# Optimization experiments

Measured on AMD Instinct MI355X. Metric: run time of the kernel, lower is better.

Reference implementation:

```python
import jax, jax.numpy as jnp
import numpy as np


def setup_inputs() -> dict:
    key = jax.random.key(0)
    k1, k2 = jax.random.split(key)
    x = jax.random.normal(k1, (32, 256, 56, 56), dtype=jnp.float32)
    # Conv2d(2 -> 1, kernel 7x7, bias=False): weight [out_c=1, in_c=2, 7, 7]
    w_conv = jax.random.normal(k2, (1, 2, 7, 7), dtype=jnp.float32) * 0.1
    return {"x": x, "w_conv": w_conv}


def reference(x, w_conv):
    # channel-wise average and max pooling -> [B, 2, H, W]
    avgout = jnp.mean(x, axis=1, keepdims=True)
    maxout = jnp.max(x, axis=1, keepdims=True)
    x1 = jnp.concatenate([avgout, maxout], axis=1)
    # 7x7 conv, padding=3 (SAME), NCHW / OIHW
    x1 = jax.lax.conv_general_dilated(
        x1, w_conv,
        window_strides=(1, 1),
        padding=((3, 3), (3, 3)),
        dimension_numbers=("NCHW", "OIHW", "NCHW"),
    )
    gate = jax.nn.sigmoid(x1)  # [B, 1, H, W]
    return x * gate
```

## Files before the change

kernel.cpp:

```cpp
#include <hip/hip_runtime.h>
#include <math.h>

#define B_    32
#define C_    256
#define H_    56
#define W_    56
#define HW_   (H_ * W_)
#define BHW_  (B_ * HW_)
#define HW4_  (HW_ / 4)
#define NF4_  (BHW_ / 4)
#define GRID_ 1568
#define CHUNKF4_ (NF4_ / GRID_)
#define POSPB_  (BHW_ / GRID_)

typedef float f4v __attribute__((ext_vector_type(4)));

__global__ __launch_bounds__(256) void sa_reduce_kernel(
    const float* __restrict__ x, float* __restrict__ pool) {
  const int t = threadIdx.x;
  const int lane = t & 15;
  const int cgrp = t >> 4;
  const unsigned if4 = (unsigned)blockIdx.x * CHUNKF4_ + lane;
  const unsigned bimg = if4 / HW4_;
  const unsigned hw4 = if4 % HW4_;
  const f4v* __restrict__ x4 = (const f4v*)x;
  const unsigned base = (bimg * C_ + cgrp) * HW4_ + hw4;

  f4v s = {0.f, 0.f, 0.f, 0.f};
  f4v m = {-INFINITY, -INFINITY, -INFINITY, -INFINITY};
#pragma unroll 8
  for (int k = 0; k < 16; ++k) {
    f4v v = x4[base + (unsigned)(k * 16) * HW4_];
    s += v;
    m = (f4v){fmaxf(m.x, v.x), fmaxf(m.y, v.y),
              fmaxf(m.z, v.z), fmaxf(m.w, v.w)};
  }

  __shared__ f4v ssum[16][16];
  __shared__ f4v smax[16][16];
  ssum[cgrp][lane] = s;
  smax[cgrp][lane] = m;
  __syncthreads();

  if (t < 16) {
    f4v S = ssum[0][t];
    f4v M = smax[0][t];
#pragma unroll
    for (int g = 1; g < 16; ++g) {
      f4v sg = ssum[g][t];
      f4v mg = smax[g][t];
      S += sg;
      M = (f4v){fmaxf(M.x, mg.x), fmaxf(M.y, mg.y),
                fmaxf(M.z, mg.z), fmaxf(M.w, mg.w)};
    }
    f4v* p4 = (f4v*)pool;
    const unsigned jf4 = (unsigned)blockIdx.x * CHUNKF4_ + t;
    const unsigned bb = jf4 / HW4_;
    const unsigned hh = jf4 % HW4_;
    p4[bb * 2 * HW4_ + hh]        = S * (1.0f / (float)C_);
    p4[bb * 2 * HW4_ + HW4_ + hh] = M;
  }
}

__global__ __launch_bounds__(256) void sa_conv_apply_kernel(
    const float* __restrict__ x, const float* __restrict__ pool,
    const float* __restrict__ wt, float* __restrict__ out) {
  const int t = threadIdx.x;
  __shared__ float partial[128];
  __shared__ f4v sgate4[CHUNKF4_];

  if (t < 2 * POSPB_) {
    const int pos = t >> 1;
    const int ic = t & 1;
    const unsigned p = (unsigned)blockIdx.x * POSPB_ + (unsigned)pos;
    const unsigned bimg = p / HW_;
    const unsigned hw = p % HW_;
    const int h = (int)(hw / W_);
    const int w = (int)(hw % W_);
    const float* pl = pool + ((long)bimg * 2 + ic) * HW_;
    const float* wr0 = wt + ic * 49;
    float acc = 0.f;
#pragma unroll
    for (int kh = 0; kh < 7; ++kh) {
      const int ih = h + kh - 3;
      if (ih < 0 || ih >= H_) continue;
      const float* row = pl + ih * W_;
      const float* wr = wr0 + kh * 7;
#pragma unroll
      for (int kw = 0; kw < 7; ++kw) {
        const int iw = w + kw - 3;
        if (iw < 0 || iw >= W_) continue;
        acc = fmaf(row[iw], wr[kw], acc);
      }
    }
    partial[t] = acc;
  }
  __syncthreads();
  if (t < POSPB_) {
    float a = partial[2 * t] + partial[2 * t + 1];
    ((float*)sgate4)[t] = 1.0f / (1.0f + __expf(-a));
  }
  __syncthreads();

  const int lane = t & 15;
  const int cgrp = t >> 4;
  const unsigned if4 = (unsigned)blockIdx.x * CHUNKF4_ + lane;
  const unsigned bimg = if4 / HW4_;
  const unsigned hw4 = if4 % HW4_;
  const unsigned base = (bimg * C_ + cgrp) * HW4_ + hw4;
  const f4v* __restrict__ x4 = (const f4v*)x;
  f4v* __restrict__ o4 = (f4v*)out;
  const f4v g = sgate4[lane];
#pragma unroll 8
  for (int k = 0; k < 16; ++k) {
    const unsigned idx = base + (unsigned)(k * 16) * HW4_;
    f4v v = x4[idx];
    __builtin_nontemporal_store(v * g, &o4[idx]);
  }
}

extern "C" void kernel_launch(void* const* d_in, const int* in_sizes, int n_in,
                              void* d_out, int out_size, void* d_ws, size_t ws_size,
                              hipStream_t stream) {
  const float* x  = (const float*)d_in[0];
  const float* wc = (const float*)d_in[1];
  float* out = (float*)d_out;
  float* pool = (float*)d_ws;

  sa_reduce_kernel<<<GRID_, 256, 0, stream>>>(x, pool);
  sa_conv_apply_kernel<<<GRID_, 256, 0, stream>>>(x, pool, wc, out);
}
```

Before: 202.3 us.

## Double block size, widen spatial chunk, split conv rows across four threads

Halves the grid and doubles threads per block, so each block covers 128 contiguous float4 positions (32 lanes) instead of 64. Each thread now walks 16 consecutive channels instead of channels strided by 16. The 7x7 conv is split over four threads per output position (two input channels times two kernel-row halves), which keeps all 512 threads busy and shortens the serial conv prologue before the apply loop. Launch bounds request 6 blocks per CU, which may constrain registers. Each wave now reads a 512-byte contiguous run per channel row, slightly shorter than the 256-byte runs... actually wider than before.

After: 208.4 us. 1.03x slower.

```diff
diff --git a/kernel.cpp b/kernel.cpp
--- a/kernel.cpp
+++ b/kernel.cpp
@@ -9,40 +9,40 @@
 #define BHW_  (B_ * HW_)
 #define HW4_  (HW_ / 4)
 #define NF4_  (BHW_ / 4)
-#define GRID_ 1568
+#define GRID_ 784
 #define CHUNKF4_ (NF4_ / GRID_)
 #define POSPB_  (BHW_ / GRID_)
 
 typedef float f4v __attribute__((ext_vector_type(4)));
 
-__global__ __launch_bounds__(256) void sa_reduce_kernel(
+__global__ __launch_bounds__(512, 6) void sa_reduce_kernel(
     const float* __restrict__ x, float* __restrict__ pool) {
   const int t = threadIdx.x;
-  const int lane = t & 15;
-  const int cgrp = t >> 4;
+  const int lane = t & 31;
+  const int cgrp = t >> 5;
   const unsigned if4 = (unsigned)blockIdx.x * CHUNKF4_ + lane;
   const unsigned bimg = if4 / HW4_;
   const unsigned hw4 = if4 % HW4_;
   const f4v* __restrict__ x4 = (const f4v*)x;
-  const unsigned base = (bimg * C_ + cgrp) * HW4_ + hw4;
+  const unsigned base = (bimg * C_ + cgrp * 16) * HW4_ + hw4;
 
   f4v s = {0.f, 0.f, 0.f, 0.f};
   f4v m = {-INFINITY, -INFINITY, -INFINITY, -INFINITY};
 #pragma unroll 8
   for (int k = 0; k < 16; ++k) {
-    f4v v = x4[base + (unsigned)(k * 16) * HW4_];
+    f4v v = x4[base + (unsigned)k * HW4_];
     s += v;
     m = (f4v){fmaxf(m.x, v.x), fmaxf(m.y, v.y),
               fmaxf(m.z, v.z), fmaxf(m.w, v.w)};
   }
 
-  __shared__ f4v ssum[16][16];
-  __shared__ f4v smax[16][16];
+  __shared__ f4v ssum[16][32];
+  __shared__ f4v smax[16][32];
   ssum[cgrp][lane] = s;
   smax[cgrp][lane] = m;
   __syncthreads();
 
-  if (t < 16) {
+  if (t < 32) {
     f4v S = ssum[0][t];
     f4v M = smax[0][t];
 #pragma unroll
@@ -62,26 +62,29 @@
   }
 }
 
-__global__ __launch_bounds__(256) void sa_conv_apply_kernel(
+__global__ __launch_bounds__(512, 6) void sa_conv_apply_kernel(
     const float* __restrict__ x, const float* __restrict__ pool,
     const float* __restrict__ wt, float* __restrict__ out) {
   const int t = threadIdx.x;
-  __shared__ float partial[128];
+  __shared__ float partial[512];
   __shared__ f4v sgate4[CHUNKF4_];
 
-  if (t < 2 * POSPB_) {
-    const int pos = t >> 1;
-    const int ic = t & 1;
+  {
+    const int pos = t >> 2;
+    const int sub = t & 3;
+    const int ic = sub & 1;
+    const int khalf = sub >> 1;
     const unsigned p = (unsigned)blockIdx.x * POSPB_ + (unsigned)pos;
-    const unsigned bimg = p / HW_;
+    const unsigned bimg_a = p / HW_;
     const unsigned hw = p % HW_;
     const int h = (int)(hw / W_);
     const int w = (int)(hw % W_);
-    const float* pl = pool + ((long)bimg * 2 + ic) * HW_;
+    const float* pl = pool + ((long)bimg_a * 2 + ic) * HW_;
     const float* wr0 = wt + ic * 49;
+    const int kh0 = khalf ? 4 : 0;
+    const int kh1 = khalf ? 7 : 4;
     float acc = 0.f;
-#pragma unroll
-    for (int kh = 0; kh < 7; ++kh) {
+    for (int kh = kh0; kh < kh1; ++kh) {
       const int ih = h + kh - 3;
       if (ih < 0 || ih >= H_) continue;
       const float* row = pl + ih * W_;
@@ -97,23 +100,24 @@
   }
   __syncthreads();
   if (t < POSPB_) {
-    float a = partial[2 * t] + partial[2 * t + 1];
+    float a = partial[4 * t] + partial[4 * t + 1] +
+              partial[4 * t + 2] + partial[4 * t + 3];
     ((float*)sgate4)[t] = 1.0f / (1.0f + __expf(-a));
   }
   __syncthreads();
 
-  const int lane = t & 15;
-  const int cgrp = t >> 4;
+  const int lane = t & 31;
+  const int cgrp = t >> 5;
   const unsigned if4 = (unsigned)blockIdx.x * CHUNKF4_ + lane;
   const unsigned bimg = if4 / HW4_;
   const unsigned hw4 = if4 % HW4_;
-  const unsigned base = (bimg * C_ + cgrp) * HW4_ + hw4;
+  const unsigned base = (bimg * C_ + cgrp * 16) * HW4_ + hw4;
   const f4v* __restrict__ x4 = (const f4v*)x;
   f4v* __restrict__ o4 = (f4v*)out;
   const f4v g = sgate4[lane];
 #pragma unroll 8
   for (int k = 0; k < 16; ++k) {
-    const unsigned idx = base + (unsigned)(k * 16) * HW4_;
+    const unsigned idx = base + (unsigned)k * HW4_;
     f4v v = x4[idx];
     __builtin_nontemporal_store(v * g, &o4[idx]);
   }
@@ -127,6 +131,6 @@
   float* out = (float*)d_out;
   float* pool = (float*)d_ws;
 
-  sa_reduce_kernel<<<GRID_, 256, 0, stream>>>(x, pool);
-  sa_conv_apply_kernel<<<GRID_, 256, 0, stream>>>(x, pool, wc, out);
+  sa_reduce_kernel<<<GRID_, 512, 0, stream>>>(x, pool);
+  sa_conv_apply_kernel<<<GRID_, 512, 0, stream>>>(x, pool, wc, out);
 }
```

## Split pooling into partial reduce, combine+conv, and contiguous apply kernels

Applied to the files above, without the earlier changes.

Replaces the two-kernel pipeline with three kernels. The first produces partial channel sums and maxes over groups of 8 channels. The second combines the partials and computes the 7x7 conv and sigmoid from shared-memory tiles. The third applies the gate using fully contiguous 4096-float4 chunks per block, with the gate map staged in LDS. The aim is to make loads coalesced and contiguous rather than strided across channels, and to stop recomputing the conv redundantly, at the cost of an extra launch and about 25 MB of partial writes and reads. It falls back to the old path if the workspace is too small.

Measured after the change: 209.2 us. 3.4% more time.

```diff
diff --git a/kernel.cpp b/kernel.cpp
--- a/kernel.cpp
+++ b/kernel.cpp
@@ -5,60 +5,200 @@
 #define C_    256
 #define H_    56
 #define W_    56
-#define HW_   (H_ * W_)
-#define BHW_  (B_ * HW_)
-#define HW4_  (HW_ / 4)
-#define NF4_  (BHW_ / 4)
-#define GRID_ 1568
-#define CHUNKF4_ (NF4_ / GRID_)
-#define POSPB_  (BHW_ / GRID_)
+#define HW_   3136
+#define HW4_  784
+#define NF4_  (B_ * C_ * HW4_)
 
 typedef float f4v __attribute__((ext_vector_type(4)));
+
+static __device__ __forceinline__ f4v f4max(f4v a, f4v b) {
+  return (f4v){fmaxf(a.x, b.x), fmaxf(a.y, b.y), fmaxf(a.z, b.z), fmaxf(a.w, b.w)};
+}
+
+
+__global__ __launch_bounds__(256, 4) void k1_partial(
+    const float* __restrict__ x, float* __restrict__ part) {
+  const int t = threadIdx.x;
+  const unsigned k = blockIdx.x;
+  const unsigned img = k >> 5;
+  const unsigned grp = k & 31u;
+  const f4v* __restrict__ x4 = (const f4v*)x;
+  f4v* __restrict__ p4 = (f4v*)part;
+  const unsigned xbase = (img * 256u + grp * 8u) * 784u;
+  const int w = t >> 6;
+  const int l = t & 63;
+
+#pragma unroll
+  for (int it = 0; it < 4; ++it) {
+    const int off = it * 64 + l;
+    if (off < 196) {
+      const unsigned q = 196u * (unsigned)w + (unsigned)off;
+      f4v v0 = x4[xbase + 0u * 784u + q];
+      f4v v1 = x4[xbase + 1u * 784u + q];
+      f4v v2 = x4[xbase + 2u * 784u + q];
+      f4v v3 = x4[xbase + 3u * 784u + q];
+      f4v v4 = x4[xbase + 4u * 784u + q];
+      f4v v5 = x4[xbase + 5u * 784u + q];
+      f4v v6 = x4[xbase + 6u * 784u + q];
+      f4v v7 = x4[xbase + 7u * 784u + q];
+      f4v s = ((v0 + v1) + (v2 + v3)) + ((v4 + v5) + (v6 + v7));
+      f4v m = f4max(f4max(f4max(v0, v1), f4max(v2, v3)),
+                    f4max(f4max(v4, v5), f4max(v6, v7)));
+      p4[k * 1568u + q]        = s;
+      p4[k * 1568u + 784u + q] = m;
+    }
+  }
+}
+
+__global__ __launch_bounds__(256) void k1b_combine_conv(
+    const float* __restrict__ part, const float* __restrict__ wt,
+    float* __restrict__ gate) {
+  const int t = threadIdx.x;
+  const unsigned blk = blockIdx.x;
+  const unsigned img = blk / 7u;
+  const int r0 = (int)(blk % 7u) * 8;
+
+  __shared__ float lsum[784];
+  __shared__ float lmax[784];
+  const f4v* __restrict__ p4 = (const f4v*)part;
+
+  for (int s = t; s < 392; s += 256) {
+    const int is_max = (s >= 196);
+    const int sl = is_max ? (s - 196) : s;
+    const int lr = sl / 14;
+    const int c  = sl % 14;
+    const int row = r0 - 3 + lr;
+    f4v acc;
+    if (row < 0 || row >= 56) {
+      acc = (f4v){0.f, 0.f, 0.f, 0.f};
+    } else {
+      const unsigned qq = (unsigned)(row * 14 + c);
+      if (!is_max) {
+        f4v a = {0.f, 0.f, 0.f, 0.f};
+#pragma unroll 8
+        for (int g = 0; g < 32; ++g)
+          a += p4[(img * 32u + (unsigned)g) * 1568u + qq];
+        acc = a * (1.0f / 256.0f);
+      } else {
+        f4v a = {-INFINITY, -INFINITY, -INFINITY, -INFINITY};
+#pragma unroll 8
+        for (int g = 0; g < 32; ++g)
+          a = f4max(a, p4[(img * 32u + (unsigned)g) * 1568u + 784u + qq]);
+        acc = a;
+      }
+    }
+    ((f4v*)(is_max ? lmax : lsum))[sl] = acc;
+  }
+  __syncthreads();
+
+  const float* __restrict__ w0 = wt;
+  const float* __restrict__ w1 = wt + 49;
+#pragma unroll
+  for (int pp = 0; pp < 2; ++pp) {
+    const int pos = t + 256 * pp;
+    if (pos < 448) {
+      const int lro = pos / 56;
+      const int wc = pos % 56;
+      float a = 0.f;
+#pragma unroll
+      for (int kh = 0; kh < 7; ++kh) {
+        const float* rs = lsum + (lro + kh) * 56;
+        const float* rm = lmax + (lro + kh) * 56;
+        const float* t0 = w0 + kh * 7;
+        const float* t1 = w1 + kh * 7;
+#pragma unroll
+        for (int kw = 0; kw < 7; ++kw) {
+          const int iw = wc + kw - 3;
+          if (iw >= 0 && iw < 56) {
+            a = fmaf(rs[iw], t0[kw], a);
+            a = fmaf(rm[iw], t1[kw], a);
+          }
+        }
+      }
+      gate[img * 3136u + (unsigned)(r0 + lro) * 56u + (unsigned)wc] =
+          1.0f / (1.0f + __expf(-a));
+    }
+  }
+}
+
+__global__ __launch_bounds__(256) void k2_apply(
+    const float* __restrict__ x, const float* __restrict__ gate,
+    float* __restrict__ out) {
+  const int t = threadIdx.x;
+  const unsigned k = blockIdx.x;
+  const unsigned img = k / 49u;
+  const unsigned S = (176u * (k % 49u)) % 784u;
+
+  __shared__ f4v lg[784];
+  const f4v* __restrict__ g4 = (const f4v*)gate;
+#pragma unroll
+  for (int it = 0; it < 4; ++it) {
+    const int idx = t + 256 * it;
+    if (idx < 784) lg[idx] = g4[img * 784u + (unsigned)idx];
+  }
+  __syncthreads();
+
+  const f4v* __restrict__ x4 = (const f4v*)x;
+  f4v* __restrict__ o4 = (f4v*)out;
+  const unsigned base = k * 4096u + (unsigned)t;
+  unsigned qc = S + (unsigned)t;
+  if (qc >= 784u) qc -= 784u;
+
+#pragma unroll
+  for (int hb = 0; hb < 2; ++hb) {
+    f4v v[8];
+#pragma unroll
+    for (int u = 0; u < 8; ++u)
+      v[u] = x4[base + (unsigned)(hb * 8 + u) * 256u];
+#pragma unroll
+    for (int u = 0; u < 8; ++u) {
+      const f4v g = lg[qc];
+      __builtin_nontemporal_store(v[u] * g,
+                                  &o4[base + (unsigned)(hb * 8 + u) * 256u]);
+      qc += 256u;
+      if (qc >= 784u) qc -= 784u;
+    }
+  }
+}
 
 __global__ __launch_bounds__(256) void sa_reduce_kernel(
     const float* __restrict__ x, float* __restrict__ pool) {
   const int t = threadIdx.x;
   const int lane = t & 15;
   const int cgrp = t >> 4;
-  const unsigned if4 = (unsigned)blockIdx.x * CHUNKF4_ + lane;
-  const unsigned bimg = if4 / HW4_;
-  const unsigned hw4 = if4 % HW4_;
-  const f4v* __restrict__ x4 = (const f4v*)x;
-  const unsigned base = (bimg * C_ + cgrp) * HW4_ + hw4;
+  const unsigned if4 = (unsigned)blockIdx.x * 16u + (unsigned)lane;
+  const unsigned bimg = if4 / 784u;
+  const unsigned hw4 = if4 % 784u;
+  const f4v* __restrict__ x4 = (const f4v*)x;
+  const unsigned base = (bimg * 256u + (unsigned)cgrp) * 784u + hw4;
 
   f4v s = {0.f, 0.f, 0.f, 0.f};
   f4v m = {-INFINITY, -INFINITY, -INFINITY, -INFINITY};
 #pragma unroll 8
-  for (int k = 0; k < 16; ++k) {
-    f4v v = x4[base + (unsigned)(k * 16) * HW4_];
+  for (int kk = 0; kk < 16; ++kk) {
+    f4v v = x4[base + (unsigned)(kk * 16) * 784u];
     s += v;
-    m = (f4v){fmaxf(m.x, v.x), fmaxf(m.y, v.y),
-              fmaxf(m.z, v.z), fmaxf(m.w, v.w)};
-  }
-
+    m = f4max(m, v);
+  }
   __shared__ f4v ssum[16][16];
   __shared__ f4v smax[16][16];
   ssum[cgrp][lane] = s;
   smax[cgrp][lane] = m;
   __syncthreads();
-
   if (t < 16) {
     f4v S = ssum[0][t];
     f4v M = smax[0][t];
 #pragma unroll
     for (int g = 1; g < 16; ++g) {
-      f4v sg = ssum[g][t];
-      f4v mg = smax[g][t];
-      S += sg;
-      M = (f4v){fmaxf(M.x, mg.x), fmaxf(M.y, mg.y),
-                fmaxf(M.z, mg.z), fmaxf(M.w, mg.w)};
+      S += ssum[g][t];
+      M = f4max(M, smax[g][t]);
     }
     f4v* p4 = (f4v*)pool;
-    const unsigned jf4 = (unsigned)blockIdx.x * CHUNKF4_ + t;
-    const unsigned bb = jf4 / HW4_;
-    const unsigned hh = jf4 % HW4_;
-    p4[bb * 2 * HW4_ + hh]        = S * (1.0f / (float)C_);
-    p4[bb * 2 * HW4_ + HW4_ + hh] = M;
+    const unsigned jf4 = (unsigned)blockIdx.x * 16u + (unsigned)t;
+    const unsigned bb = jf4 / 784u;
+    const unsigned hh = jf4 % 784u;
+    p4[bb * 1568u + hh]        = S * (1.0f / 256.0f);
+    p4[bb * 1568u + 784u + hh] = M;
   }
 }
 
@@ -67,36 +207,35 @@
     const float* __restrict__ wt, float* __restrict__ out) {
   const int t = threadIdx.x;
   __shared__ float partial[128];
-  __shared__ f4v sgate4[CHUNKF4_];
-
-  if (t < 2 * POSPB_) {
+  __shared__ f4v sgate4[16];
+  if (t < 128) {
     const int pos = t >> 1;
     const int ic = t & 1;
-    const unsigned p = (unsigned)blockIdx.x * POSPB_ + (unsigned)pos;
-    const unsigned bimg = p / HW_;
-    const unsigned hw = p % HW_;
-    const int h = (int)(hw / W_);
-    const int w = (int)(hw % W_);
-    const float* pl = pool + ((long)bimg * 2 + ic) * HW_;
+    const unsigned p = (unsigned)blockIdx.x * 64u + (unsigned)pos;
+    const unsigned bimg = p / 3136u;
+    const unsigned hw = p % 3136u;
+    const int h = (int)(hw / 56u);
+    const int w = (int)(hw % 56u);
+    const float* pl = pool + ((long)bimg * 2 + ic) * 3136;
     const float* wr0 = wt + ic * 49;
     float acc = 0.f;
 #pragma unroll
     for (int kh = 0; kh < 7; ++kh) {
       const int ih = h + kh - 3;
-      if (ih < 0 || ih >= H_) continue;
-      const float* row = pl + ih * W_;
+      if (ih < 0 || ih >= 56) continue;
+      const float* row = pl + ih * 56;
       const float* wr = wr0 + kh * 7;
 #pragma unroll
       for (int kw = 0; kw < 7; ++kw) {
         const int iw = w + kw - 3;
-        if (iw < 0 || iw >= W_) continue;
+        if (iw < 0 || iw >= 56) continue;
         acc = fmaf(row[iw], wr[kw], acc);
       }
     }
     partial[t] = acc;
   }
   __syncthreads();
-  if (t < POSPB_) {
+  if (t < 64) {
     float a = partial[2 * t] + partial[2 * t + 1];
     ((float*)sgate4)[t] = 1.0f / (1.0f + __expf(-a));
   }
@@ -104,16 +243,16 @@
 
   const int lane = t & 15;
   const int cgrp = t >> 4;
-  const unsigned if4 = (unsigned)blockIdx.x * CHUNKF4_ + lane;
-  const unsigned bimg = if4 / HW4_;
-  const unsigned hw4 = if4 % HW4_;
-  const unsigned base = (bimg * C_ + cgrp) * HW4_ + hw4;
+  const unsigned if4 = (unsigned)blockIdx.x * 16u + (unsigned)lane;
+  const unsigned bimg = if4 / 784u;
+  const unsigned hw4 = if4 % 784u;
+  const unsigned base = (bimg * 256u + (unsigned)cgrp) * 784u + hw4;
   const f4v* __restrict__ x4 = (const f4v*)x;
   f4v* __restrict__ o4 = (f4v*)out;
   const f4v g = sgate4[lane];
 #pragma unroll 8
-  for (int k = 0; k < 16; ++k) {
-    const unsigned idx = base + (unsigned)(k * 16) * HW4_;
+  for (int kk = 0; kk < 16; ++kk) {
+    const unsigned idx = base + (unsigned)(kk * 16) * 784u;
     f4v v = x4[idx];
     __builtin_nontemporal_store(v * g, &o4[idx]);
   }
@@ -125,8 +264,20 @@
   const float* x  = (const float*)d_in[0];
   const float* wc = (const float*)d_in[1];
   float* out = (float*)d_out;
-  float* pool = (float*)d_ws;
-
-  sa_reduce_kernel<<<GRID_, 256, 0, stream>>>(x, pool);
-  sa_conv_apply_kernel<<<GRID_, 256, 0, stream>>>(x, pool, wc, out);
-}
+
+  const size_t PART_F4 = 1024u * 1568u;
+  const size_t GATE_F4 = 32u * 784u;
+  const size_t NEED = (PART_F4 + GATE_F4) * 16u;
+
+  if (ws_size >= NEED) {
+    float* part = (float*)d_ws;
+    float* gate = (float*)d_ws + PART_F4 * 4;
+    k1_partial<<<1024, 256, 0, stream>>>(x, part);
+    k1b_combine_conv<<<224, 256, 0, stream>>>(part, wc, gate);
+    k2_apply<<<1568, 256, 0, stream>>>(x, gate, out);
+  } else {
+    float* pool = (float*)d_ws;
+    sa_reduce_kernel<<<1568, 256, 0, stream>>>(x, pool);
+    sa_conv_apply_kernel<<<1568, 256, 0, stream>>>(x, pool, wc, out);
+  }
+}
```
